# Performance work log

Measured on AMD Instinct MI355X. Metric: run time of the kernel, lower is better.

Reference implementation:

```python
import jax, jax.numpy as jnp
import numpy as np
import math

B, S, D, H, L, F, V, C = 8, 1024, 768, 12, 6, 3072, 32000, 10
DK = D // H
EPS = 1e-5


def _pos_encoding(seq_len, d):
    pos = jnp.arange(seq_len, dtype=jnp.float32)[:, None]
    div = jnp.exp(jnp.arange(0, d, 2, dtype=jnp.float32) * (-math.log(10000.0) / d))
    pe = jnp.zeros((seq_len, d), dtype=jnp.float32)
    pe = pe.at[:, 0::2].set(jnp.sin(pos * div))
    pe = pe.at[:, 1::2].set(jnp.cos(pos * div))
    return pe


def _layernorm(x, scale, bias):
    mu = jnp.mean(x, axis=-1, keepdims=True)
    var = jnp.mean(jnp.square(x - mu), axis=-1, keepdims=True)
    return (x - mu) * jax.lax.rsqrt(var + EPS) * scale + bias


def setup_inputs() -> dict:
    key = jax.random.key(0)
    ks = jax.random.split(key, 14)
    s = 0.02
    return {
        "tokens": jax.random.randint(ks[0], (B, S), 0, V),
        "emb": jax.random.normal(ks[1], (V, D), jnp.float32) * s,
        "Wq": jax.random.normal(ks[2], (L, D, D), jnp.float32) * s,
        "Wk": jax.random.normal(ks[3], (L, D, D), jnp.float32) * s,
        "Wv": jax.random.normal(ks[4], (L, D, D), jnp.float32) * s,
        "Wo": jax.random.normal(ks[5], (L, D, D), jnp.float32) * s,
        "W1": jax.random.normal(ks[6], (L, D, F), jnp.float32) * s,
        "W2": jax.random.normal(ks[7], (L, F, D), jnp.float32) * s,
        "ln1_s": jnp.ones((L, D), jnp.float32),
        "ln1_b": jnp.zeros((L, D), jnp.float32),
        "ln2_s": jnp.ones((L, D), jnp.float32),
        "ln2_b": jnp.zeros((L, D), jnp.float32),
        "Wc": jax.random.normal(ks[8], (D, C), jnp.float32) * s,
        "bc": jnp.zeros((C,), jnp.float32),
    }


def _block(x, p):
    Wq, Wk, Wv, Wo, W1, W2, l1s, l1b, l2s, l2b = p
    b, s = x.shape[0], x.shape[1]
    q = (x @ Wq).reshape(b, s, H, DK)
    k = (x @ Wk).reshape(b, s, H, DK)
    v = (x @ Wv).reshape(b, s, H, DK)
    scores = jnp.einsum("bqhd,bkhd->bhqk", q, k) / math.sqrt(DK)
    attn = jax.nn.softmax(scores, axis=-1)
    out = jnp.einsum("bhqk,bkhd->bqhd", attn, v).reshape(b, s, D) @ Wo
    x = _layernorm(x + out, l1s, l1b)
    ffn = jax.nn.relu(x @ W1) @ W2
    x = _layernorm(x + ffn, l2s, l2b)
    return x


def reference(tokens, emb, Wq, Wk, Wv, Wo, W1, W2, ln1_s, ln1_b, ln2_s, ln2_b, Wc, bc):
    x = emb[tokens] + _pos_encoding(tokens.shape[1], D)[None]

    def step(h, p):
        return _block(h, p), None

    x, _ = jax.lax.scan(step, x, (Wq, Wk, Wv, Wo, W1, W2, ln1_s, ln1_b, ln2_s, ln2_b))
    pooled = jnp.mean(x, axis=1)  # [B, D]
    return pooled @ Wc + bc
```

## Files before the change

### kernel.cpp

```cpp
#include <hip/hip_runtime.h>
#include <hip/hip_bf16.h>
#include <math.h>

#define BB 8
#define SS 1024
#define DD 768
#define HH 12
#define LL 6
#define FF 3072
#define CC 10
#define BS_ (BB * SS)

typedef __attribute__((ext_vector_type(8))) short short8v;
typedef __attribute__((ext_vector_type(4))) float f32x4;
typedef __attribute__((ext_vector_type(8))) unsigned short ushort8v;
typedef __attribute__((ext_vector_type(4))) unsigned short ushort4v;
typedef __attribute__((ext_vector_type(2))) unsigned int uint2v;

__device__ inline unsigned short f2bf(float f) {
  unsigned int u = __builtin_bit_cast(unsigned int, f);
  u += 0x7fffu + ((u >> 16) & 1u);
  return (unsigned short)(u >> 16);
}
__device__ inline float bf2f(unsigned short u) {
  return __builtin_bit_cast(float, (unsigned int)u << 16);
}
__device__ inline unsigned int pack_bf2(float lo, float hi) {
  unsigned int a = __builtin_bit_cast(unsigned int, lo);
  unsigned int b = __builtin_bit_cast(unsigned int, hi);
  a += 0x7fffu + ((a >> 16) & 1u);
  b += 0x7fffu + ((b >> 16) & 1u);
  return __builtin_amdgcn_perm(b, a, 0x07060302u);
}
__device__ inline void gload16(const void* g, void* l) {
  __builtin_amdgcn_global_load_lds((const __attribute__((address_space(1))) void*)g,
                                   (__attribute__((address_space(3))) void*)l, 16, 0, 0);
}

__device__ inline float wave_sum(float v) {
#pragma unroll
  for (int off = 32; off > 0; off >>= 1) v += __shfl_down(v, off);
  return v;
}
__device__ inline float block_sum(float v, float* red) {
  int t = threadIdx.x;
  v = wave_sum(v);
  __syncthreads();
  if ((t & 63) == 0) red[t >> 6] = v;
  __syncthreads();
  return red[0] + red[1] + red[2] + red[3];
}

__global__ __launch_bounds__(256) void k_embed(const int* __restrict__ tokens,
                                               const float* __restrict__ emb,
                                               float* __restrict__ x,
                                               ushort* __restrict__ xb) {
  int row = blockIdx.x;
  int s = row & (SS - 1);
  int tok = tokens[row];
  const float* e = emb + (size_t)tok * DD;
  float* xr = x + (size_t)row * DD;
  ushort* xbr = xb + (size_t)row * DD;
  for (int d = threadIdx.x; d < DD; d += 256) {
    float freq = expf((float)(d & ~1) * -0.0119926306f);
    float ang = (float)s * freq;
    float pe = (d & 1) ? cosf(ang) : sinf(ang);
    float v = e[d] + pe;
    xr[d] = v;
    xbr[d] = f2bf(v);
  }
}

__global__ __launch_bounds__(256) void k_transpose_all(
    const float* __restrict__ wq, const float* __restrict__ wk,
    const float* __restrict__ wv, const float* __restrict__ wo,
    const float* __restrict__ w1, const float* __restrict__ w2,
    ushort* __restrict__ wqkv_t, ushort* __restrict__ wo_t,
    ushort* __restrict__ w1_t, ushort* __restrict__ w2_t) {
  __shared__ float tile[32][33];
  int bid = blockIdx.x;
  const float* W; ushort* Wt; int K, N, lb;
  if (bid < 1728) {
    int m = bid / 576; lb = bid - m * 576;
    W = (m == 0) ? wq : (m == 1) ? wk : wv;
    Wt = wqkv_t + m * 768 * 768; K = 768; N = 768;
  } else if (bid < 2304) {
    W = wo; Wt = wo_t; K = 768; N = 768; lb = bid - 1728;
  } else if (bid < 4608) {
    W = w1; Wt = w1_t; K = 768; N = 3072; lb = bid - 2304;
  } else {
    W = w2; Wt = w2_t; K = 3072; N = 768; lb = bid - 4608;
  }
  int nbk = K >> 5;
  int k0 = (lb % nbk) * 32, n0 = (lb / nbk) * 32;
  int t = threadIdx.x;
  int r = t >> 3, c4 = (t & 7) * 4;
  float4 v = *(const float4*)(W + (size_t)(k0 + r) * N + n0 + c4);
  tile[r][c4 + 0] = v.x; tile[r][c4 + 1] = v.y;
  tile[r][c4 + 2] = v.z; tile[r][c4 + 3] = v.w;
  __syncthreads();
  ushort4v o;
#pragma unroll
  for (int i = 0; i < 4; ++i) o[i] = f2bf(tile[c4 + i][r]);
  *(ushort4v*)(Wt + (size_t)(n0 + r) * K + k0 + c4) = o;
}

template <int RELU, int TN>
__global__ __launch_bounds__(256) void k_gemm_db(const ushort* __restrict__ A,
                                                 const ushort* __restrict__ Bt,
                                                 ushort* __restrict__ Cout,
                                                 int M, int N, int K) {
  constexpr int NF = TN / 32;
  __shared__ ushort smem[2][(128 + TN) * 64];
  int bidl = blockIdx.y * gridDim.x + blockIdx.x;
  int nwg = gridDim.x * gridDim.y;
  int cpx = nwg >> 3;
  int tid = (bidl & 7) * cpx + (bidl >> 3);
  int n0 = (tid % gridDim.x) * TN, m0 = (tid / gridDim.x) * 128;
  int t = threadIdx.x, w = t >> 6, l = t & 63;
  int wr = (w >> 1) * 64, wc = (w & 1) * (TN / 2);
  int lr = l & 15, lg = l >> 4;
  f32x4 acc[4][NF] = {};
  int sr8 = l >> 3;
  int scw = ((l & 7) ^ sr8) * 8;
  const ushort* ag = A + (size_t)(m0 + w * 8 + sr8) * K + scw;
  const ushort* bg = Bt + (size_t)(n0 + w * 8 + sr8) * K + scw;
  int nk = K >> 6;
  {
    ushort* al = &smem[0][(w * 8) * 64];
    ushort* bl = &smem[0][128 * 64 + (w * 8) * 64];
#pragma unroll
    for (int ii = 0; ii < 4; ++ii) gload16(ag + (size_t)ii * 32 * K, al + ii * 2048);
#pragma unroll
    for (int ii = 0; ii < TN / 32; ++ii) gload16(bg + (size_t)ii * 32 * K, bl + ii * 2048);
  }
  int rsw = lr & 7;
  for (int k = 0; k < nk; ++k) {
    __syncthreads();
    if (k + 1 < nk) {
      int kb = (k + 1) & 1;
      int kc0 = (k + 1) * 64;
      ushort* al = &smem[kb][(w * 8) * 64];
      ushort* bl = &smem[kb][128 * 64 + (w * 8) * 64];
#pragma unroll
      for (int ii = 0; ii < 4; ++ii) gload16(ag + (size_t)ii * 32 * K + kc0, al + ii * 2048);
#pragma unroll
      for (int ii = 0; ii < TN / 32; ++ii) gload16(bg + (size_t)ii * 32 * K + kc0, bl + ii * 2048);
    }
    const ushort* As = &smem[k & 1][0];
    const ushort* Bs = &smem[k & 1][128 * 64];
#pragma unroll
    for (int ks = 0; ks < 2; ++ks) {
      short8v af[4], bfr[NF];
#pragma unroll
      for (int mi = 0; mi < 4; ++mi)
        af[mi] = *(const short8v*)(As + (wr + mi * 16 + lr) * 64 + (((ks * 4 + lg) ^ rsw) << 3));
#pragma unroll
      for (int ni = 0; ni < NF; ++ni)
        bfr[ni] = *(const short8v*)(Bs + (wc + ni * 16 + lr) * 64 + (((ks * 4 + lg) ^ rsw) << 3));
      __builtin_amdgcn_s_setprio(1);
#pragma unroll
      for (int mi = 0; mi < 4; ++mi)
#pragma unroll
        for (int ni = 0; ni < NF; ++ni)
          acc[mi][ni] = __builtin_amdgcn_mfma_f32_16x16x32_bf16(af[mi], bfr[ni], acc[mi][ni], 0, 0, 0);
      __builtin_amdgcn_s_setprio(0);
    }
  }
  __syncthreads();
  ushort* cst = &smem[0][0];
#pragma unroll
  for (int mi = 0; mi < 4; ++mi)
#pragma unroll
    for (int ni = 0; ni < NF; ++ni) {
      int cl = wc + ni * 16 + lr;
#pragma unroll
      for (int i = 0; i < 4; ++i) {
        int rl = wr + mi * 16 + lg * 4 + i;
        float v = acc[mi][ni][i];
        if (RELU) v = fmaxf(v, 0.f);
        cst[rl * TN + (cl ^ (((rl >> 2) & 3) << 4))] = f2bf(v);
      }
    }
  __syncthreads();
  {
    int row = t >> 1, half = t & 1;
    int swr = ((row >> 2) & 3) << 4;
    ushort* crow = Cout + (size_t)(m0 + row) * N + n0 + half * (TN / 2);
#pragma unroll
    for (int c8 = 0; c8 < TN / 16; ++c8) {
      int c = half * (TN / 2) + c8 * 8;
      ushort8v vv = *(const ushort8v*)(&cst[row * TN + (c ^ swr)]);
      *(ushort8v*)(crow + c8 * 8) = vv;
    }
  }
}

__global__ __launch_bounds__(256) void k_flash(const ushort* __restrict__ qkv,
                                               ushort* __restrict__ ao) {
  __shared__ ushort Ks[64][64];
  __shared__ ushort Vt[64][64];
  __shared__ ushort Ps[4][32][64];
  const int LD = 2304;
  int bidl = blockIdx.y * gridDim.x + blockIdx.x;
  int tid = (bidl & 7) * 96 + (bidl >> 3);
  int qt = tid & 7;
  int bh = tid >> 3;
  int h = bh % HH, b = bh / HH;
  int t = threadIdx.x, w = t >> 6, l = t & 63;
  int lr = l & 15, lg = l >> 4;
  int sw = (l & 7) << 3;
  int q0 = qt * 128;
  const ushort* qbase = qkv + (size_t)(b * SS) * LD + h * 64;
  const ushort* kbase = qbase + 768;
  const ushort* vbase = qbase + 1536;
  short8v qf[2][2];
#pragma unroll
  for (int qg = 0; qg < 2; ++qg) {
    const ushort* qrow = qbase + (size_t)(q0 + w * 32 + qg * 16 + lr) * LD + lg * 8;
    qf[qg][0] = *(const short8v*)(qrow);
    qf[qg][1] = *(const short8v*)(qrow + 32);
  }
  const float CEXP = 0.125f * 1.44269504f;
  float l_run[2] = {0.f, 0.f};
  f32x4 o_acc[2][4] = {};
  int krow_ = w * 16 + (l >> 3);
  int kcol_ = ((l & 7) * 8) ^ ((krow_ & 7) << 3);
  const ushort* kg = kbase + (size_t)krow_ * LD + kcol_;
  ushort* kl = &Ks[w * 16][0];
  int d_ = t & 7;
  int dk0 = d_ * 8;
  int kv2 = (t >> 3) * 2;
  for (int kt = 0; kt < 16; ++kt) {
    int kv0 = kt * 64;
    const ushort* vr0 = vbase + (size_t)(kv0 + kv2) * LD + dk0;
    ushort8v v0 = *(const ushort8v*)(vr0);
    ushort8v v1 = *(const ushort8v*)(vr0 + LD);
    __syncthreads();
    gload16(kg + (size_t)kv0 * LD, kl);
    gload16(kg + (size_t)(kv0 + 8) * LD, kl + 512);
#pragma unroll
    for (int i = 0; i < 8; ++i) {
      unsigned int pack = (unsigned int)v0[i] | ((unsigned int)v1[i] << 16);
      *(unsigned int*)(&Vt[dk0 + i][kv2 ^ (((i ^ d_) & 7) << 3)]) = pack;
    }
    __syncthreads();
    short8v kf[4][2];
#pragma unroll
    for (int mi = 0; mi < 4; ++mi) {
      int kvr = mi * 16 + lr;
      kf[mi][0] = *(const short8v*)(&Ks[kvr][(lg * 8) ^ sw]);
      kf[mi][1] = *(const short8v*)(&Ks[kvr][(32 + lg * 8) ^ sw]);
    }
    f32x4 s[2][4] = {};
    __builtin_amdgcn_s_setprio(1);
#pragma unroll
    for (int mi = 0; mi < 4; ++mi)
#pragma unroll
      for (int qg = 0; qg < 2; ++qg) {
        s[qg][mi] = __builtin_amdgcn_mfma_f32_16x16x32_bf16(kf[mi][0], qf[qg][0], s[qg][mi], 0, 0, 0);
        s[qg][mi] = __builtin_amdgcn_mfma_f32_16x16x32_bf16(kf[mi][1], qf[qg][1], s[qg][mi], 0, 0, 0);
      }
    __builtin_amdgcn_s_setprio(0);
#pragma unroll
    for (int qg = 0; qg < 2; ++qg) {
      float psum = 0.f;
#pragma unroll
      for (int mi = 0; mi < 4; ++mi) {
        float p0 = exp2f(s[qg][mi][0] * CEXP);
        float p1 = exp2f(s[qg][mi][1] * CEXP);
        float p2 = exp2f(s[qg][mi][2] * CEXP);
        float p3 = exp2f(s[qg][mi][3] * CEXP);
        psum += (p0 + p1) + (p2 + p3);
        uint2v pp;
        pp.x = pack_bf2(p0, p1);
        pp.y = pack_bf2(p2, p3);
        *(uint2v*)(&Ps[w][qg * 16 + lr][(mi * 16 + lg * 4) ^ ((lr & 7) << 3)]) = pp;
      }
      psum += __shfl_xor(psum, 16);
      psum += __shfl_xor(psum, 32);
      l_run[qg] += psum;
    }
#pragma unroll
    for (int ks = 0; ks < 2; ++ks) {
      short8v pf[2];
      pf[0] = *(const short8v*)(&Ps[w][lr][(ks * 32 + lg * 8) ^ sw]);
      pf[1] = *(const short8v*)(&Ps[w][16 + lr][(ks * 32 + lg * 8) ^ sw]);
      short8v vf[4];
#pragma unroll
      for (int mi = 0; mi < 4; ++mi) {
        int swz = ((lr & 7) ^ (mi * 2 + (lr >> 3))) & 7;
        vf[mi] = *(const short8v*)(&Vt[mi * 16 + lr][(ks * 32 + lg * 8) ^ (swz << 3)]);
      }
      __builtin_amdgcn_s_setprio(1);
#pragma unroll
      for (int mi = 0; mi < 4; ++mi)
#pragma unroll
        for (int qg = 0; qg < 2; ++qg)
          o_acc[qg][mi] = __builtin_amdgcn_mfma_f32_16x16x32_bf16(vf[mi], pf[qg], o_acc[qg][mi], 0, 0, 0);
      __builtin_amdgcn_s_setprio(0);
    }
  }
#pragma unroll
  for (int qg = 0; qg < 2; ++qg) {
    float invl = 1.f / l_run[qg];
    ushort* orow = ao + (size_t)(b * SS + q0 + w * 32 + qg * 16 + lr) * DD + h * 64;
#pragma unroll
    for (int mi = 0; mi < 4; ++mi) {
      ushort4v o;
#pragma unroll
      for (int i = 0; i < 4; ++i) o[i] = f2bf(o_acc[qg][mi][i] * invl);
      *(ushort4v*)(orow + mi * 16 + lg * 4) = o;
    }
  }
}

__global__ __launch_bounds__(256) void k_addln(float* __restrict__ x,
                                               ushort* __restrict__ xb,
                                               const ushort* __restrict__ y,
                                               const float* __restrict__ sc,
                                               const float* __restrict__ bi) {
  __shared__ float red[4];
  int row = blockIdx.x, t = threadIdx.x;
  float* xr = x + (size_t)row * DD;
  ushort* xbr = xb + (size_t)row * DD;
  const ushort* yr = y + (size_t)row * DD;
  float vals[3];
  float s = 0.f;
#pragma unroll
  for (int i = 0; i < 3; ++i) {
    float vv = xr[t + 256 * i] + bf2f(yr[t + 256 * i]);
    vals[i] = vv;
    s += vv;
  }
  float mu = block_sum(s, red) * (1.f / 768.f);
  float vs = 0.f;
#pragma unroll
  for (int i = 0; i < 3; ++i) {
    float c = vals[i] - mu;
    vs += c * c;
  }
  float rstd = rsqrtf(block_sum(vs, red) * (1.f / 768.f) + 1e-5f);
#pragma unroll
  for (int i = 0; i < 3; ++i) {
    int d = t + 256 * i;
    float o = (vals[i] - mu) * rstd * sc[d] + bi[d];
    xr[d] = o;
    xbr[d] = f2bf(o);
  }
}

__global__ __launch_bounds__(256) void k_pool(const float* __restrict__ x,
                                              float* __restrict__ pooled) {
  int b = blockIdx.x, chunk = blockIdx.y, t = threadIdx.x;
  float a0 = 0, a1 = 0, a2 = 0;
  for (int s2 = chunk * 128; s2 < chunk * 128 + 128; ++s2) {
    const float* xr = x + (size_t)(b * SS + s2) * DD;
    a0 += xr[t]; a1 += xr[t + 256]; a2 += xr[t + 512];
  }
  atomicAdd(&pooled[b * DD + t], a0 * (1.f / 1024.f));
  atomicAdd(&pooled[b * DD + t + 256], a1 * (1.f / 1024.f));
  atomicAdd(&pooled[b * DD + t + 512], a2 * (1.f / 1024.f));
}

__global__ __launch_bounds__(64) void k_cls(const float* __restrict__ pooled,
                                            const float* __restrict__ Wc,
                                            const float* __restrict__ bc,
                                            float* __restrict__ out) {
  int idx = blockIdx.x;
  int b = idx / CC, c = idx % CC;
  int t = threadIdx.x;
  float acc = 0.f;
  for (int d0 = t; d0 < DD; d0 += 64) acc = fmaf(pooled[b * DD + d0], Wc[d0 * CC + c], acc);
  acc = wave_sum(acc);
  if (t == 0) out[b * CC + c] = acc + bc[c];
}

extern "C" void kernel_launch(void* const* d_in, const int* in_sizes, int n_in,
                              void* d_out, int out_size, void* d_ws, size_t ws_size,
                              hipStream_t stream) {
  (void)in_sizes; (void)n_in; (void)out_size; (void)ws_size;
  const int* tokens = (const int*)d_in[0];
  const float* emb = (const float*)d_in[1];
  const float* Wq = (const float*)d_in[2];
  const float* Wk = (const float*)d_in[3];
  const float* Wv = (const float*)d_in[4];
  const float* Wo = (const float*)d_in[5];
  const float* W1 = (const float*)d_in[6];
  const float* W2 = (const float*)d_in[7];
  const float* l1s = (const float*)d_in[8];
  const float* l1b = (const float*)d_in[9];
  const float* l2s = (const float*)d_in[10];
  const float* l2b = (const float*)d_in[11];
  const float* Wc = (const float*)d_in[12];
  const float* bc = (const float*)d_in[13];
  float* out = (float*)d_out;

  char* p = (char*)d_ws;
  float* x = (float*)p;                 p += (size_t)BS_ * DD * 4;
  ushort* xb = (ushort*)p;              p += (size_t)BS_ * DD * 2;
  ushort* qkvb = (ushort*)p;
  ushort* hb = (ushort*)p;
  ushort* ao = (ushort*)(p + (size_t)BS_ * 2304 * 2);
  p += (size_t)BS_ * FF * 2;
  ushort* yb = (ushort*)p;              p += (size_t)BS_ * DD * 2;
  ushort* wt = (ushort*)p;              p += (size_t)(2304 * 768 + 768 * 768 + 3072 * 768 + 768 * 3072) * 2;
  float* pooled = (float*)p;

  ushort* wqkv_t = wt;
  ushort* wo_t = wqkv_t + 2304 * 768;
  ushort* w1_t = wo_t + 768 * 768;
  ushort* w2_t = w1_t + 3072 * 768;

  k_embed<<<BS_, 256, 0, stream>>>(tokens, emb, x, xb);

  for (int l = 0; l < LL; ++l) {
    k_transpose_all<<<6912, 256, 0, stream>>>(
        Wq + (size_t)l * DD * DD, Wk + (size_t)l * DD * DD,
        Wv + (size_t)l * DD * DD, Wo + (size_t)l * DD * DD,
        W1 + (size_t)l * DD * FF, W2 + (size_t)l * FF * DD,
        wqkv_t, wo_t, w1_t, w2_t);

    k_gemm_db<0, 128><<<dim3(2304 / 128, BS_ / 128), 256, 0, stream>>>(xb, wqkv_t, qkvb, BS_, 2304, DD);
    k_flash<<<dim3(SS / 128, BB * HH), 256, 0, stream>>>(qkvb, ao);
    k_gemm_db<0, 64><<<dim3(DD / 64, BS_ / 128), 256, 0, stream>>>(ao, wo_t, yb, BS_, DD, DD);
    k_addln<<<BS_, 256, 0, stream>>>(x, xb, yb, l1s + l * DD, l1b + l * DD);
    k_gemm_db<1, 128><<<dim3(FF / 128, BS_ / 128), 256, 0, stream>>>(xb, w1_t, hb, BS_, FF, DD);
    k_gemm_db<0, 64><<<dim3(DD / 64, BS_ / 128), 256, 0, stream>>>(hb, w2_t, yb, BS_, DD, FF);
    k_addln<<<BS_, 256, 0, stream>>>(x, xb, yb, l2s + l * DD, l2b + l * DD);
  }

  hipMemsetAsync(pooled, 0, (size_t)BB * DD * sizeof(float), stream);
  k_pool<<<dim3(BB, 8), 256, 0, stream>>>(x, pooled);
  k_cls<<<BB * CC, 64, 0, stream>>>(pooled, Wc, bc, out);
}
```

Measured before the change: 1.487 ms.

## Rewrite flash attention with 32x32 MFMA, register-resident P and double-buffered K/V

The attention kernel moves from 16x16x32 to 32x32x16 bf16 MFMAs. The softmax probabilities stay in registers, converted with v_cvt_pk_bf16 and rearranged with permlane32_swap, so the per-wave LDS round trip for P is gone. K/V tiles are double-buffered in LDS so the next tile's loads overlap the current compute, which saves one barrier per iteration. The output goes through an LDS tile for wide coalesced stores. The cost is higher register pressure and reliance on gfx950-specific instructions.

```diff
diff --git a/kernel.cpp b/kernel.cpp
--- a/kernel.cpp
+++ b/kernel.cpp
@@ -13,9 +13,10 @@
 
 typedef __attribute__((ext_vector_type(8))) short short8v;
 typedef __attribute__((ext_vector_type(4))) float f32x4;
+typedef __attribute__((ext_vector_type(16))) float f32x16;
 typedef __attribute__((ext_vector_type(8))) unsigned short ushort8v;
 typedef __attribute__((ext_vector_type(4))) unsigned short ushort4v;
-typedef __attribute__((ext_vector_type(2))) unsigned int uint2v;
+typedef __attribute__((ext_vector_type(4))) unsigned int uint4v;
 
 __device__ inline unsigned short f2bf(float f) {
   unsigned int u = __builtin_bit_cast(unsigned int, f);
@@ -25,12 +26,13 @@
 __device__ inline float bf2f(unsigned short u) {
   return __builtin_bit_cast(float, (unsigned int)u << 16);
 }
-__device__ inline unsigned int pack_bf2(float lo, float hi) {
-  unsigned int a = __builtin_bit_cast(unsigned int, lo);
-  unsigned int b = __builtin_bit_cast(unsigned int, hi);
-  a += 0x7fffu + ((a >> 16) & 1u);
-  b += 0x7fffu + ((b >> 16) & 1u);
-  return __builtin_amdgcn_perm(b, a, 0x07060302u);
+__device__ inline unsigned int cvtpk(float lo, float hi) {
+  unsigned int r;
+  asm("v_cvt_pk_bf16_f32 %0, %1, %2" : "=v"(r) : "v"(lo), "v"(hi));
+  return r;
+}
+__device__ inline void plswap(unsigned int& a, unsigned int& b) {
+  asm volatile("v_permlane32_swap_b32 %0, %1" : "+v"(a), "+v"(b));
 }
 __device__ inline void gload16(const void* g, void* l) {
   __builtin_amdgcn_global_load_lds((const __attribute__((address_space(1))) void*)g,
@@ -198,119 +200,138 @@
 
 __global__ __launch_bounds__(256) void k_flash(const ushort* __restrict__ qkv,
                                                ushort* __restrict__ ao) {
-  __shared__ ushort Ks[64][64];
-  __shared__ ushort Vt[64][64];
-  __shared__ ushort Ps[4][32][64];
+  __shared__ ushort Ks[2][64][64];
+  __shared__ ushort Vt[2][64][64];
   const int LD = 2304;
   int bidl = blockIdx.y * gridDim.x + blockIdx.x;
   int tid = (bidl & 7) * 96 + (bidl >> 3);
   int qt = tid & 7;
   int bh = tid >> 3;
-  int h = bh % HH, b = bh / HH;
+  int hd = bh % HH, b = bh / HH;
   int t = threadIdx.x, w = t >> 6, l = t & 63;
-  int lr = l & 15, lg = l >> 4;
-  int sw = (l & 7) << 3;
+  int q = l & 31, hl = l >> 5;
   int q0 = qt * 128;
-  const ushort* qbase = qkv + (size_t)(b * SS) * LD + h * 64;
+  const ushort* qbase = qkv + (size_t)(b * SS) * LD + hd * 64;
   const ushort* kbase = qbase + 768;
   const ushort* vbase = qbase + 1536;
-  short8v qf[2][2];
-#pragma unroll
-  for (int qg = 0; qg < 2; ++qg) {
-    const ushort* qrow = qbase + (size_t)(q0 + w * 32 + qg * 16 + lr) * LD + lg * 8;
-    qf[qg][0] = *(const short8v*)(qrow);
-    qf[qg][1] = *(const short8v*)(qrow + 32);
+  short8v qfb[4];
+  {
+    const ushort* qrow = qbase + (size_t)(q0 + w * 32 + q) * LD + hl * 8;
+    qfb[0] = *(const short8v*)(qrow);
+    qfb[1] = *(const short8v*)(qrow + 16);
+    qfb[2] = *(const short8v*)(qrow + 32);
+    qfb[3] = *(const short8v*)(qrow + 48);
   }
   const float CEXP = 0.125f * 1.44269504f;
-  float l_run[2] = {0.f, 0.f};
-  f32x4 o_acc[2][4] = {};
+  float l_run = 0.f;
+  f32x16 o_acc[2] = {};
   int krow_ = w * 16 + (l >> 3);
   int kcol_ = ((l & 7) * 8) ^ ((krow_ & 7) << 3);
   const ushort* kg = kbase + (size_t)krow_ * LD + kcol_;
-  ushort* kl = &Ks[w * 16][0];
   int d_ = t & 7;
   int dk0 = d_ * 8;
   int kv2 = (t >> 3) * 2;
+  const ushort* vg = vbase + (size_t)kv2 * LD + dk0;
+  {
+    gload16(kg, &Ks[0][w * 16][0]);
+    gload16(kg + (size_t)8 * LD, &Ks[0][w * 16 + 8][0]);
+    ushort8v v0 = *(const ushort8v*)(vg);
+    ushort8v v1 = *(const ushort8v*)(vg + LD);
+#pragma unroll
+    for (int i = 0; i < 8; ++i) {
+      unsigned int pk = (unsigned int)v0[i] | ((unsigned int)v1[i] << 16);
+      *(unsigned int*)(&Vt[0][dk0 + i][kv2 ^ (((i ^ d_) & 7) << 3)]) = pk;
+    }
+  }
   for (int kt = 0; kt < 16; ++kt) {
-    int kv0 = kt * 64;
-    const ushort* vr0 = vbase + (size_t)(kv0 + kv2) * LD + dk0;
-    ushort8v v0 = *(const ushort8v*)(vr0);
-    ushort8v v1 = *(const ushort8v*)(vr0 + LD);
+    int cur = kt & 1, nxt = cur ^ 1;
     __syncthreads();
-    gload16(kg + (size_t)kv0 * LD, kl);
-    gload16(kg + (size_t)(kv0 + 8) * LD, kl + 512);
-#pragma unroll
-    for (int i = 0; i < 8; ++i) {
-      unsigned int pack = (unsigned int)v0[i] | ((unsigned int)v1[i] << 16);
-      *(unsigned int*)(&Vt[dk0 + i][kv2 ^ (((i ^ d_) & 7) << 3)]) = pack;
-    }
-    __syncthreads();
-    short8v kf[4][2];
-#pragma unroll
-    for (int mi = 0; mi < 4; ++mi) {
-      int kvr = mi * 16 + lr;
-      kf[mi][0] = *(const short8v*)(&Ks[kvr][(lg * 8) ^ sw]);
-      kf[mi][1] = *(const short8v*)(&Ks[kvr][(32 + lg * 8) ^ sw]);
-    }
-    f32x4 s[2][4] = {};
+    ushort8v v0n, v1n;
+    if (kt < 15) {
+      const ushort* kgn = kg + (size_t)(kt + 1) * 64 * LD;
+      gload16(kgn, &Ks[nxt][w * 16][0]);
+      gload16(kgn + (size_t)8 * LD, &Ks[nxt][w * 16 + 8][0]);
+      const ushort* vgn = vg + (size_t)(kt + 1) * 64 * LD;
+      v0n = *(const ushort8v*)(vgn);
+      v1n = *(const ushort8v*)(vgn + LD);
+    }
+    f32x16 s[2] = {};
     __builtin_amdgcn_s_setprio(1);
 #pragma unroll
-    for (int mi = 0; mi < 4; ++mi)
-#pragma unroll
-      for (int qg = 0; qg < 2; ++qg) {
-        s[qg][mi] = __builtin_amdgcn_mfma_f32_16x16x32_bf16(kf[mi][0], qf[qg][0], s[qg][mi], 0, 0, 0);
-        s[qg][mi] = __builtin_amdgcn_mfma_f32_16x16x32_bf16(kf[mi][1], qf[qg][1], s[qg][mi], 0, 0, 0);
+    for (int c = 0; c < 4; ++c)
+#pragma unroll
+      for (int mi = 0; mi < 2; ++mi) {
+        short8v kf = *(const short8v*)(
+            &Ks[cur][mi * 32 + q][(((c << 1) | hl) ^ (l & 7)) << 3]);
+        s[mi] = __builtin_amdgcn_mfma_f32_32x32x16_bf16(kf, qfb[c], s[mi], 0, 0, 0);
       }
     __builtin_amdgcn_s_setprio(0);
-#pragma unroll
-    for (int qg = 0; qg < 2; ++qg) {
-      float psum = 0.f;
-#pragma unroll
-      for (int mi = 0; mi < 4; ++mi) {
-        float p0 = exp2f(s[qg][mi][0] * CEXP);
-        float p1 = exp2f(s[qg][mi][1] * CEXP);
-        float p2 = exp2f(s[qg][mi][2] * CEXP);
-        float p3 = exp2f(s[qg][mi][3] * CEXP);
-        psum += (p0 + p1) + (p2 + p3);
-        uint2v pp;
-        pp.x = pack_bf2(p0, p1);
-        pp.y = pack_bf2(p2, p3);
-        *(uint2v*)(&Ps[w][qg * 16 + lr][(mi * 16 + lg * 4) ^ ((lr & 7) << 3)]) = pp;
-      }
-      psum += __shfl_xor(psum, 16);
-      psum += __shfl_xor(psum, 32);
-      l_run[qg] += psum;
-    }
-#pragma unroll
-    for (int ks = 0; ks < 2; ++ks) {
-      short8v pf[2];
-      pf[0] = *(const short8v*)(&Ps[w][lr][(ks * 32 + lg * 8) ^ sw]);
-      pf[1] = *(const short8v*)(&Ps[w][16 + lr][(ks * 32 + lg * 8) ^ sw]);
-      short8v vf[4];
-#pragma unroll
-      for (int mi = 0; mi < 4; ++mi) {
-        int swz = ((lr & 7) ^ (mi * 2 + (lr >> 3))) & 7;
-        vf[mi] = *(const short8v*)(&Vt[mi * 16 + lr][(ks * 32 + lg * 8) ^ (swz << 3)]);
-      }
-      __builtin_amdgcn_s_setprio(1);
-#pragma unroll
-      for (int mi = 0; mi < 4; ++mi)
-#pragma unroll
-        for (int qg = 0; qg < 2; ++qg)
-          o_acc[qg][mi] = __builtin_amdgcn_mfma_f32_16x16x32_bf16(vf[mi], pf[qg], o_acc[qg][mi], 0, 0, 0);
-      __builtin_amdgcn_s_setprio(0);
-    }
-  }
-#pragma unroll
-  for (int qg = 0; qg < 2; ++qg) {
-    float invl = 1.f / l_run[qg];
-    ushort* orow = ao + (size_t)(b * SS + q0 + w * 32 + qg * 16 + lr) * DD + h * 64;
-#pragma unroll
-    for (int mi = 0; mi < 4; ++mi) {
-      ushort4v o;
-#pragma unroll
-      for (int i = 0; i < 4; ++i) o[i] = f2bf(o_acc[qg][mi][i] * invl);
-      *(ushort4v*)(orow + mi * 16 + lg * 4) = o;
+    float p[2][16];
+    float psum = 0.f;
+#pragma unroll
+    for (int mi = 0; mi < 2; ++mi)
+#pragma unroll
+      for (int r = 0; r < 16; ++r) {
+        float e = exp2f(s[mi][r] * CEXP);
+        p[mi][r] = e;
+        psum += e;
+      }
+    psum += __shfl_xor(psum, 32);
+    l_run += psum;
+    short8v pfb[4];
+#pragma unroll
+    for (int mi = 0; mi < 2; ++mi)
+#pragma unroll
+      for (int k2 = 0; k2 < 2; ++k2) {
+        unsigned int a0 = cvtpk(p[mi][8 * k2 + 0], p[mi][8 * k2 + 1]);
+        unsigned int a1 = cvtpk(p[mi][8 * k2 + 2], p[mi][8 * k2 + 3]);
+        unsigned int b0 = cvtpk(p[mi][8 * k2 + 4], p[mi][8 * k2 + 5]);
+        unsigned int b1 = cvtpk(p[mi][8 * k2 + 6], p[mi][8 * k2 + 7]);
+        plswap(a0, b0);
+        plswap(a1, b1);
+        uint4v u;
+        u[0] = a0; u[1] = a1; u[2] = b0; u[3] = b1;
+        pfb[mi * 2 + k2] = __builtin_bit_cast(short8v, u);
+      }
+    if (kt < 15) {
+#pragma unroll
+      for (int i = 0; i < 8; ++i) {
+        unsigned int pk = (unsigned int)v0n[i] | ((unsigned int)v1n[i] << 16);
+        *(unsigned int*)(&Vt[nxt][dk0 + i][kv2 ^ (((i ^ d_) & 7) << 3)]) = pk;
+      }
+    }
+    __builtin_amdgcn_s_setprio(1);
+#pragma unroll
+    for (int ks = 0; ks < 4; ++ks)
+#pragma unroll
+      for (int od = 0; od < 2; ++od) {
+        int vsw = ((l & 7) ^ ((od * 4) | ((l >> 3) & 3))) & 7;
+        short8v vf = *(const short8v*)(
+            &Vt[cur][od * 32 + q][(((ks << 1) | hl) ^ vsw) << 3]);
+        o_acc[od] = __builtin_amdgcn_mfma_f32_32x32x16_bf16(vf, pfb[ks], o_acc[od], 0, 0, 0);
+      }
+    __builtin_amdgcn_s_setprio(0);
+  }
+  __syncthreads();
+  float invl = 1.f / l_run;
+  ushort* otile = &Ks[0][0][0] + w * 2048;
+#pragma unroll
+  for (int od = 0; od < 2; ++od)
+#pragma unroll
+    for (int r = 0; r < 16; r += 2) {
+      unsigned int pk = cvtpk(o_acc[od][r] * invl, o_acc[od][r + 1] * invl);
+      int c = od * 32 + 8 * (r >> 2) + 4 * hl + (r & 3);
+      *(unsigned int*)(&otile[q * 64 + (c ^ ((q & 7) << 3))]) = pk;
+    }
+  __syncthreads();
+  {
+    int r2 = l >> 1, hf = l & 1;
+    ushort* orow = ao + (size_t)(b * SS + q0 + w * 32 + r2) * DD + hd * 64 + hf * 32;
+#pragma unroll
+    for (int k = 0; k < 4; ++k) {
+      int c = hf * 32 + k * 8;
+      ushort8v vv = *(const ushort8v*)(&otile[r2 * 64 + (c ^ ((r2 & 7) << 3))]);
+      *(ushort8v*)(orow + k * 8) = vv;
     }
   }
 }
```

Result: slower. 1.527 ms (+2.7%).

## Drop fp32 residual stream, use bf16 residual and single-wave LayerNorm, fold softmax scale into Q

Applied to the files above, without the earlier changes.

Removes the fp32 copy of the residual stream, so embed, add+LayerNorm and pooling read and write only the bf16 activations. This cuts global memory traffic in the add+LN kernels. LayerNorm is rewritten as a 64-thread, one-wave-per-row kernel with vectorized loads and shuffle-only reductions, which removes the shared-memory block reductions and their barriers. The softmax scale and log2e factor are applied to Q in the QKV GEMM epilogue, which drops a multiply per score in the flash kernel. The trade-off is lower precision: the residual is now re-rounded to bf16 every layer, and Q is rounded after scaling.

```diff
diff --git a/kernel.cpp b/kernel.cpp
--- a/kernel.cpp
+++ b/kernel.cpp
@@ -17,6 +17,8 @@
 typedef __attribute__((ext_vector_type(4))) unsigned short ushort4v;
 typedef __attribute__((ext_vector_type(2))) unsigned int uint2v;
 
+#define CEXPQ 0.18033688f
+
 __device__ inline unsigned short f2bf(float f) {
   unsigned int u = __builtin_bit_cast(unsigned int, f);
   u += 0x7fffu + ((u >> 16) & 1u);
@@ -42,32 +44,20 @@
   for (int off = 32; off > 0; off >>= 1) v += __shfl_down(v, off);
   return v;
 }
-__device__ inline float block_sum(float v, float* red) {
-  int t = threadIdx.x;
-  v = wave_sum(v);
-  __syncthreads();
-  if ((t & 63) == 0) red[t >> 6] = v;
-  __syncthreads();
-  return red[0] + red[1] + red[2] + red[3];
-}
 
 __global__ __launch_bounds__(256) void k_embed(const int* __restrict__ tokens,
                                                const float* __restrict__ emb,
-                                               float* __restrict__ x,
                                                ushort* __restrict__ xb) {
   int row = blockIdx.x;
   int s = row & (SS - 1);
   int tok = tokens[row];
   const float* e = emb + (size_t)tok * DD;
-  float* xr = x + (size_t)row * DD;
   ushort* xbr = xb + (size_t)row * DD;
   for (int d = threadIdx.x; d < DD; d += 256) {
     float freq = expf((float)(d & ~1) * -0.0119926306f);
     float ang = (float)s * freq;
     float pe = (d & 1) ? cosf(ang) : sinf(ang);
-    float v = e[d] + pe;
-    xr[d] = v;
-    xbr[d] = f2bf(v);
+    xbr[d] = f2bf(e[d] + pe);
   }
 }
 
@@ -105,7 +95,7 @@
   *(ushort4v*)(Wt + (size_t)(n0 + r) * K + k0 + c4) = o;
 }
 
-template <int RELU, int TN>
+template <int RELU, int TN, int SCALEQ = 0>
 __global__ __launch_bounds__(256) void k_gemm_db(const ushort* __restrict__ A,
                                                  const ushort* __restrict__ Bt,
                                                  ushort* __restrict__ Cout,
@@ -168,6 +158,7 @@
     }
   }
   __syncthreads();
+  float osc = (SCALEQ && n0 < 768) ? CEXPQ : 1.0f;
   ushort* cst = &smem[0][0];
 #pragma unroll
   for (int mi = 0; mi < 4; ++mi)
@@ -179,6 +170,7 @@
         int rl = wr + mi * 16 + lg * 4 + i;
         float v = acc[mi][ni][i];
         if (RELU) v = fmaxf(v, 0.f);
+        if (SCALEQ) v *= osc;
         cst[rl * TN + (cl ^ (((rl >> 2) & 3) << 4))] = f2bf(v);
       }
     }
@@ -221,7 +213,6 @@
     qf[qg][0] = *(const short8v*)(qrow);
     qf[qg][1] = *(const short8v*)(qrow + 32);
   }
-  const float CEXP = 0.125f * 1.44269504f;
   float l_run[2] = {0.f, 0.f};
   f32x4 o_acc[2][4] = {};
   int krow_ = w * 16 + (l >> 3);
@@ -267,10 +258,10 @@
       float psum = 0.f;
 #pragma unroll
       for (int mi = 0; mi < 4; ++mi) {
-        float p0 = exp2f(s[qg][mi][0] * CEXP);
-        float p1 = exp2f(s[qg][mi][1] * CEXP);
-        float p2 = exp2f(s[qg][mi][2] * CEXP);
-        float p3 = exp2f(s[qg][mi][3] * CEXP);
+        float p0 = exp2f(s[qg][mi][0]);
+        float p1 = exp2f(s[qg][mi][1]);
+        float p2 = exp2f(s[qg][mi][2]);
+        float p3 = exp2f(s[qg][mi][3]);
         psum += (p0 + p1) + (p2 + p3);
         uint2v pp;
         pp.x = pack_bf2(p0, p1);
@@ -315,48 +306,64 @@
   }
 }
 
-__global__ __launch_bounds__(256) void k_addln(float* __restrict__ x,
-                                               ushort* __restrict__ xb,
-                                               const ushort* __restrict__ y,
-                                               const float* __restrict__ sc,
-                                               const float* __restrict__ bi) {
-  __shared__ float red[4];
-  int row = blockIdx.x, t = threadIdx.x;
-  float* xr = x + (size_t)row * DD;
-  ushort* xbr = xb + (size_t)row * DD;
+__global__ __launch_bounds__(64) void k_addln(ushort* __restrict__ xb,
+                                              const ushort* __restrict__ y,
+                                              const float* __restrict__ sc,
+                                              const float* __restrict__ bi) {
+  int row = blockIdx.x, l = threadIdx.x;
+  int d0 = l * 12;
+  ushort* xr = xb + (size_t)row * DD;
   const ushort* yr = y + (size_t)row * DD;
-  float vals[3];
+  ushort4v xa[3], ya[3];
+#pragma unroll
+  for (int j = 0; j < 3; ++j) {
+    xa[j] = *(const ushort4v*)(xr + d0 + j * 4);
+    ya[j] = *(const ushort4v*)(yr + d0 + j * 4);
+  }
+  float v[12];
   float s = 0.f;
 #pragma unroll
-  for (int i = 0; i < 3; ++i) {
-    float vv = xr[t + 256 * i] + bf2f(yr[t + 256 * i]);
-    vals[i] = vv;
-    s += vv;
-  }
-  float mu = block_sum(s, red) * (1.f / 768.f);
+  for (int j = 0; j < 3; ++j)
+#pragma unroll
+    for (int i = 0; i < 4; ++i) {
+      float vv = bf2f(xa[j][i]) + bf2f(ya[j][i]);
+      v[j * 4 + i] = vv;
+      s += vv;
+    }
+  float mu = wave_sum(s);
+  mu = __shfl(mu, 0) * (1.f / 768.f);
   float vs = 0.f;
 #pragma unroll
-  for (int i = 0; i < 3; ++i) {
-    float c = vals[i] - mu;
+  for (int i = 0; i < 12; ++i) {
+    float c = v[i] - mu;
     vs += c * c;
   }
-  float rstd = rsqrtf(block_sum(vs, red) * (1.f / 768.f) + 1e-5f);
-#pragma unroll
-  for (int i = 0; i < 3; ++i) {
-    int d = t + 256 * i;
-    float o = (vals[i] - mu) * rstd * sc[d] + bi[d];
-    xr[d] = o;
-    xbr[d] = f2bf(o);
-  }
-}
-
-__global__ __launch_bounds__(256) void k_pool(const float* __restrict__ x,
+  vs = wave_sum(vs);
+  float rstd = rsqrtf(__shfl(vs, 0) * (1.f / 768.f) + 1e-5f);
+  float4 scv[3], biv[3];
+#pragma unroll
+  for (int j = 0; j < 3; ++j) {
+    scv[j] = *(const float4*)(sc + d0 + j * 4);
+    biv[j] = *(const float4*)(bi + d0 + j * 4);
+  }
+#pragma unroll
+  for (int j = 0; j < 3; ++j) {
+    ushort4v o;
+    const float* sj = (const float*)&scv[j];
+    const float* bj = (const float*)&biv[j];
+#pragma unroll
+    for (int i = 0; i < 4; ++i) o[i] = f2bf((v[j * 4 + i] - mu) * rstd * sj[i] + bj[i]);
+    *(ushort4v*)(xr + d0 + j * 4) = o;
+  }
+}
+
+__global__ __launch_bounds__(256) void k_pool(const ushort* __restrict__ xb,
                                               float* __restrict__ pooled) {
   int b = blockIdx.x, chunk = blockIdx.y, t = threadIdx.x;
   float a0 = 0, a1 = 0, a2 = 0;
   for (int s2 = chunk * 128; s2 < chunk * 128 + 128; ++s2) {
-    const float* xr = x + (size_t)(b * SS + s2) * DD;
-    a0 += xr[t]; a1 += xr[t + 256]; a2 += xr[t + 512];
+    const ushort* xr = xb + (size_t)(b * SS + s2) * DD;
+    a0 += bf2f(xr[t]); a1 += bf2f(xr[t + 256]); a2 += bf2f(xr[t + 512]);
   }
   atomicAdd(&pooled[b * DD + t], a0 * (1.f / 1024.f));
   atomicAdd(&pooled[b * DD + t + 256], a1 * (1.f / 1024.f));
@@ -397,7 +404,6 @@
   float* out = (float*)d_out;
 
   char* p = (char*)d_ws;
-  float* x = (float*)p;                 p += (size_t)BS_ * DD * 4;
   ushort* xb = (ushort*)p;              p += (size_t)BS_ * DD * 2;
   ushort* qkvb = (ushort*)p;
   ushort* hb = (ushort*)p;
@@ -412,7 +418,7 @@
   ushort* w1_t = wo_t + 768 * 768;
   ushort* w2_t = w1_t + 3072 * 768;
 
-  k_embed<<<BS_, 256, 0, stream>>>(tokens, emb, x, xb);
+  k_embed<<<BS_, 256, 0, stream>>>(tokens, emb, xb);
 
   for (int l = 0; l < LL; ++l) {
     k_transpose_all<<<6912, 256, 0, stream>>>(
@@ -421,16 +427,16 @@
         W1 + (size_t)l * DD * FF, W2 + (size_t)l * FF * DD,
         wqkv_t, wo_t, w1_t, w2_t);
 
-    k_gemm_db<0, 128><<<dim3(2304 / 128, BS_ / 128), 256, 0, stream>>>(xb, wqkv_t, qkvb, BS_, 2304, DD);
-    k_flash<<<dim3(SS / 128, BB * HH), 256, 0, stream>>>(qkvb, ao);
+    k_gemm_db<0, 128, 1><<<dim3(2304 / 128, BS_ / 128), 256, 0, stream>>>(xb, wqkv_t, qkvb, BS_, 2304, DD);
+    k_flash<<<dim3(8, BB * HH), 256, 0, stream>>>(qkvb, ao);
     k_gemm_db<0, 64><<<dim3(DD / 64, BS_ / 128), 256, 0, stream>>>(ao, wo_t, yb, BS_, DD, DD);
-    k_addln<<<BS_, 256, 0, stream>>>(x, xb, yb, l1s + l * DD, l1b + l * DD);
+    k_addln<<<BS_, 64, 0, stream>>>(xb, yb, l1s + l * DD, l1b + l * DD);
     k_gemm_db<1, 128><<<dim3(FF / 128, BS_ / 128), 256, 0, stream>>>(xb, w1_t, hb, BS_, FF, DD);
     k_gemm_db<0, 64><<<dim3(DD / 64, BS_ / 128), 256, 0, stream>>>(hb, w2_t, yb, BS_, DD, FF);
-    k_addln<<<BS_, 256, 0, stream>>>(x, xb, yb, l2s + l * DD, l2b + l * DD);
+    k_addln<<<BS_, 64, 0, stream>>>(xb, yb, l2s + l * DD, l2b + l * DD);
   }
 
   hipMemsetAsync(pooled, 0, (size_t)BB * DD * sizeof(float), stream);
-  k_pool<<<dim3(BB, 8), 256, 0, stream>>>(x, pooled);
+  k_pool<<<dim3(BB, 8), 256, 0, stream>>>(xb, pooled);
   k_cls<<<BB * CC, 64, 0, stream>>>(pooled, Wc, bc, out);
 }
```

Result: faster. 1.430 ms (-3.8%).
